# Kernel optimization log

Hardware: AMD Instinct MI355X
Metric: run time of the kernel (lower is better)

## Reference

```python
import jax, jax.numpy as jnp
import numpy as np

B, C, N = 8, 512, 4096
G = 8          # GroupNorm groups (8 <= C)
EPS = 1e-6


def setup_inputs() -> dict:
    key = jax.random.key(0)
    ks = jax.random.split(key, 5)
    return {
        "x": jax.random.normal(ks[0], (B, C, N), dtype=jnp.float32),
        "qkv_w": jax.random.normal(ks[1], (3 * C, C), dtype=jnp.float32) * (C ** -0.5),
        "qkv_b": jax.random.normal(ks[2], (3 * C,), dtype=jnp.float32) * 0.02,
        "proj_w": jax.random.normal(ks[3], (C, C), dtype=jnp.float32) * (C ** -0.5),
        "proj_b": jax.random.normal(ks[4], (C,), dtype=jnp.float32) * 0.02,
        "gn_scale": jnp.ones((C,), dtype=jnp.float32),
        "gn_bias": jnp.zeros((C,), dtype=jnp.float32),
    }


def group_norm(x, scale, bias):
    b, c, n = x.shape
    xr = x.reshape(b, G, c // G, n)
    mean = xr.mean(axis=(2, 3), keepdims=True)
    var = xr.var(axis=(2, 3), keepdims=True)
    h = ((xr - mean) * jax.lax.rsqrt(var + EPS)).reshape(b, c, n)
    return h * scale[None, :, None] + bias[None, :, None]


def reference(x, qkv_w, qkv_b, proj_w, proj_b, gn_scale, gn_bias):
    c = x.shape[1]
    h = group_norm(x, gn_scale, gn_bias)
    # 1x1 Conv1d == channel-mixing GEMM
    qkv = jnp.einsum('oc,bcn->bon', qkv_w, h) + qkv_b[None, :, None]
    q, k, v = jnp.split(qkv, 3, axis=1)           # each [B, C, N]
    q = q * (c ** -0.5)
    k = jax.nn.softmax(k, axis=-1)                # softmax over tokens
    # linear attention: context = k v^T over tokens, then project q
    context = jnp.einsum('bdn,ben->bde', k, v)    # [B, C, C]
    out = jnp.einsum('bde,bdn->ben', context, q)  # [B, C, N]
    y = jnp.einsum('oc,bcn->bon', proj_w, out) + proj_b[None, :, None]
    return x + y
```

## Files before the change

### kernel.cpp

```cpp
#include <hip/hip_runtime.h>

#define BB 8
#define CC 512
#define NT 4096
#define GG 8
#define CPG 64
#define EPSF 1e-6f
#define SQK 0.04419417382415922f

typedef __attribute__((ext_vector_type(8))) short bf16x8;
typedef __attribute__((ext_vector_type(4))) float f32x4;

#define OFF_RED  0
#define OFF_PB2  4096
#define OFF_IZ   270336
#define OFF_WKV  274432
#define OFF_PWB  536576
#define OFF_WQT  667648
#define OFF_MB   798720
#define OFF_PBF  1847296
#define OFF_CTXB 2895872
#define OFF_PCTX 3944448
#define OFF_HT   12333056
#define OFF_KVB  20721664

__device__ __forceinline__ ushort f2bf(float f) {
  union { float f; uint u; } v; v.f = f;
  uint r = (v.u + 0x7fffu + ((v.u >> 16) & 1u)) >> 16;
  return (ushort)r;
}
__device__ __forceinline__ float bf2f(ushort h) {
  union { uint u; float f; } v; v.u = ((uint)h) << 16;
  return v.f;
}
__device__ __forceinline__ uint pk(float a, float b) {
  return (uint)f2bf(a) | ((uint)f2bf(b) << 16);
}
__device__ __forceinline__ void gload16(const ushort* g, ushort* l) {
  __builtin_amdgcn_global_load_lds((const __attribute__((address_space(1))) void*)g,
                                   (__attribute__((address_space(3))) void*)l, 16, 0, 0);
}
#define KSWZ(kofs, row) ((kofs) ^ ((((row) >> 1) & 3) << 3))

__global__ __launch_bounds__(256) void gn_stats1(const float* __restrict__ x,
                                                 float* __restrict__ red) {
  int bg = blockIdx.y, chunk = blockIdx.x;
  const float4* p4 = (const float4*)(x + (size_t)bg * (CPG * NT) + (size_t)chunk * 32768);
  int tid = threadIdx.x;
  float s = 0.f, sq = 0.f;
  for (int i = tid; i < 8192; i += 256) {
    float4 v = p4[i];
    s  += v.x + v.y + v.z + v.w;
    sq += v.x * v.x + v.y * v.y + v.z * v.z + v.w * v.w;
  }
  for (int off = 32; off > 0; off >>= 1) {
    s  += __shfl_down(s, off);
    sq += __shfl_down(sq, off);
  }
  __shared__ float ls[4], lq[4];
  int wid = tid >> 6, lane = tid & 63;
  if (lane == 0) { ls[wid] = s; lq[wid] = sq; }
  __syncthreads();
  if (tid == 0) {
    red[(bg * 8 + chunk) * 2]     = ls[0] + ls[1] + ls[2] + ls[3];
    red[(bg * 8 + chunk) * 2 + 1] = lq[0] + lq[1] + lq[2] + lq[3];
  }
}

__global__ __launch_bounds__(256) void wconv2(const float* __restrict__ qkv_w,
                                              const float* __restrict__ proj_w,
                                              ushort* __restrict__ wkvb,
                                              ushort* __restrict__ pwb) {
  int bid = blockIdx.x;
  if (bid < 512) {
    int idx = (bid * 256 + threadIdx.x) * 4;
    float4 v = *(const float4*)(qkv_w + (size_t)CC * CC + idx);
    *(uint2*)(wkvb + idx) = make_uint2(pk(v.x, v.y), pk(v.z, v.w));
  } else {
    int idx = ((bid - 512) * 256 + threadIdx.x) * 4;
    float4 v = *(const float4*)(proj_w + idx);
    *(uint2*)(pwb + idx) = make_uint2(pk(v.x, v.y), pk(v.z, v.w));
  }
}

__global__ __launch_bounds__(256) void wqt_kernel(const float* __restrict__ qkv_w,
                                                  ushort* __restrict__ wqT) {
  __shared__ float t[32][33];
  int d0 = blockIdx.y * 32, c0 = blockIdx.x * 32;
  int tid = threadIdx.x;
  int r = tid >> 3, c4 = (tid & 7) * 4;
  float4 v = *(const float4*)(qkv_w + (size_t)(d0 + r) * CC + c0 + c4);
  t[r][c4] = v.x; t[r][c4 + 1] = v.y; t[r][c4 + 2] = v.z; t[r][c4 + 3] = v.w;
  __syncthreads();
  int r2 = tid >> 3, d4 = (tid & 7) * 4;
  uint w0 = pk(t[d4][r2], t[d4 + 1][r2]);
  uint w1 = pk(t[d4 + 2][r2], t[d4 + 3][r2]);
  *(uint2*)&wqT[(size_t)(c0 + r2) * CC + d0 + d4] = make_uint2(w0, w1);
}

__global__ __launch_bounds__(256) void ht_kernel(
    const float* __restrict__ x, const float* __restrict__ red,
    const float* __restrict__ gn_scale, const float* __restrict__ gn_bias,
    ushort* __restrict__ hT) {
  __shared__ float ts[64][68];
  __shared__ float la[64], lb[64];
  int b = blockIdx.z, g = blockIdx.y, n0 = blockIdx.x * 64;
  int c0 = g * 64;
  int tid = threadIdx.x;
  if (tid == 0) {
    int bg = b * 8 + g;
    float s = 0.f, sq = 0.f;
#pragma unroll
    for (int i = 0; i < 8; i++) {
      s  += red[(bg * 8 + i) * 2];
      sq += red[(bg * 8 + i) * 2 + 1];
    }
    float mean = s / (float)(CPG * NT);
    float var  = sq / (float)(CPG * NT) - mean * mean;
    ts[0][0] = mean; ts[0][1] = rsqrtf(var + EPSF);
  }
  __syncthreads();
  if (tid < 64) {
    float mean = ts[0][0], rstd = ts[0][1];
    float a = gn_scale[c0 + tid] * rstd;
    la[tid] = a;
    lb[tid] = gn_bias[c0 + tid] - mean * a;
  }
  __syncthreads();
  int tn = (tid & 15) * 4, tc = tid >> 4;
#pragma unroll
  for (int it = 0; it < 4; it++) {
    int c = tc + it * 16;
    float a  = la[c];
    float bb = lb[c];
    float4 v = *(const float4*)(x + ((size_t)(b * CC + c0 + c)) * NT + n0 + tn);
    ts[c][tn]     = a * v.x + bb;
    ts[c][tn + 1] = a * v.y + bb;
    ts[c][tn + 2] = a * v.z + bb;
    ts[c][tn + 3] = a * v.w + bb;
  }
  __syncthreads();
#pragma unroll
  for (int it = 0; it < 2; it++) {
    int idx = tid + it * 256;
    int n = idx >> 3, c8 = (idx & 7) * 8;
    uint w[4];
#pragma unroll
    for (int j = 0; j < 4; j++)
      w[j] = pk(ts[c8 + 2 * j][n], ts[c8 + 2 * j + 1][n]);
    *(uint4*)&hT[((size_t)b * NT + n0 + n) * CC + c0 + c8] = make_uint4(w[0], w[1], w[2], w[3]);
  }
}

#define TBUF 16384

__device__ __forceinline__ void stage256(const ushort* __restrict__ G, ushort* L,
                                         int LD, int wave, int lane) {
  int rw = wave * 8 + (lane >> 3);
  int cg = lane & 7;
#pragma unroll
  for (int s = 0; s < 4; s++) {
    int row = s * 64 + rw;
    int gcol = (cg ^ (row & 7)) * 8;
    gload16(G + (size_t)row * LD + gcol, L + s * 4096 + wave * 512);
  }
}

template <int NTILES>
__device__ __forceinline__ void mfma256(const ushort* __restrict__ A,
                                        const ushort* __restrict__ B,
                                        int LDA, int LDB, ushort* As, ushort* Bs,
                                        int tid, f32x4 acc[8][4]) {
  int wave = tid >> 6, lane = tid & 63;
  int wr = wave >> 2, wc = wave & 3;
  stage256(A, As, LDA, wave, lane);
  stage256(B, Bs, LDB, wave, lane);
  const ushort* gA = A + 64;
  const ushort* gB = B + 64;
  int rowA = wr * 128 + (lane & 15);
  int rowB = wc * 64 + (lane & 15);
  int kg0 = lane >> 4;
#pragma unroll 1
  for (int t = 0; t < NTILES; t++) {
    __builtin_amdgcn_s_barrier();
    asm volatile("" ::: "memory");
    if (t + 1 < NTILES) {
      stage256(gA, As + ((t + 1) & 1) * TBUF, LDA, wave, lane);
      stage256(gB, Bs + ((t + 1) & 1) * TBUF, LDB, wave, lane);
      gA += 64; gB += 64;
      asm volatile("s_waitcnt vmcnt(8)" ::: "memory");
    } else {
      asm volatile("s_waitcnt vmcnt(0)" ::: "memory");
    }
    __builtin_amdgcn_s_barrier();
    asm volatile("" ::: "memory");
    const ushort* Ab = As + (t & 1) * TBUF;
    const ushort* Bb = Bs + (t & 1) * TBUF;
#pragma unroll
    for (int kk = 0; kk < 2; kk++) {
      int kg = kg0 + kk * 4;
      bf16x8 bfr[4];
#pragma unroll
      for (int ni = 0; ni < 4; ni++) {
        int r = rowB + ni * 16;
        bfr[ni] = *(const bf16x8*)(Bb + r * 64 + ((kg ^ (r & 7)) << 3));
      }
#pragma unroll
      for (int mi = 0; mi < 8; mi++) {
        int r = rowA + mi * 16;
        bf16x8 afr = *(const bf16x8*)(Ab + r * 64 + ((kg ^ (r & 7)) << 3));
#pragma unroll
        for (int ni = 0; ni < 4; ni++)
          acc[mi][ni] = __builtin_amdgcn_mfma_f32_16x16x32_bf16(afr, bfr[ni], acc[mi][ni], 0, 0, 0);
      }
    }
  }
}

template <int KTOT, int LDA, int LDB>
__device__ __forceinline__ void mfma_loop64(const ushort* __restrict__ A,
                                            const ushort* __restrict__ B,
                                            ushort* As, ushort* Bs, int tid,
                                            f32x4 acc[2][2]) {
  int wave = tid >> 6, lane = tid & 63;
  int srow = tid >> 2;
  int kofs = KSWZ((tid & 3) * 8, srow & 15);
  const ushort* ga = A + (size_t)srow * LDA + kofs;
  const ushort* gb = B + (size_t)srow * LDB + kofs;
  int lo = wave * 512;
  int wm = (wave >> 1) * 32, wn = (wave & 1) * 32;
  int rowl = lane & 15;
  int kread = KSWZ((lane >> 4) * 8, rowl);
  int aoff = (wm + rowl) * 32 + kread;
  int boff = (wn + rowl) * 32 + kread;
  constexpr int NIT = KTOT / 32;
  gload16(ga, As + lo); gload16(gb, Bs + lo);
  ga += 32; gb += 32;
#pragma unroll 1
  for (int t = 0; t < NIT; t++) {
    int cb = (t & 1) * 2048;
    int nb = 2048 - cb;
    if (t + 1 < NIT) {
      gload16(ga, As + nb + lo); gload16(gb, Bs + nb + lo);
      ga += 32; gb += 32;
      asm volatile("s_waitcnt vmcnt(2)" ::: "memory");
    } else {
      asm volatile("s_waitcnt vmcnt(0)" ::: "memory");
    }
    __builtin_amdgcn_s_barrier();
    asm volatile("" ::: "memory");
    bf16x8 a[2], b[2];
#pragma unroll
    for (int m = 0; m < 2; m++) a[m] = *(const bf16x8*)(As + cb + aoff + m * 512);
#pragma unroll
    for (int n = 0; n < 2; n++) b[n] = *(const bf16x8*)(Bs + cb + boff + n * 512);
#pragma unroll
    for (int m = 0; m < 2; m++)
#pragma unroll
      for (int n = 0; n < 2; n++)
        acc[m][n] = __builtin_amdgcn_mfma_f32_16x16x32_bf16(a[m], b[n], acc[m][n], 0, 0, 0);
    asm volatile("" ::: "memory");
    __builtin_amdgcn_s_barrier();
    asm volatile("" ::: "memory");
  }
}

__global__ __launch_bounds__(512) void kv_gemm_bf16(
    const ushort* __restrict__ wkvb, const ushort* __restrict__ hT,
    const float* __restrict__ qkv_b, ushort* __restrict__ kvb) {
  extern __shared__ ushort lds[];
  ushort* As = lds;
  ushort* Bs = lds + 2 * TBUF;
  int b = blockIdx.z, n0 = blockIdx.x * 256, m0 = blockIdx.y * 256;
  int tid = threadIdx.x;
  f32x4 acc[8][4] = {{{0.f, 0.f, 0.f, 0.f}}};
  mfma256<8>(wkvb + (size_t)m0 * CC, hT + (size_t)b * NT * CC + (size_t)n0 * CC,
             CC, CC, As, Bs, tid, acc);
  int wave = tid >> 6, lane = tid & 63;
  int wr = wave >> 2, wc = wave & 3;
  int col = lane & 15, rb = (lane >> 4) * 4;
  bool isK = (m0 < 512);
#pragma unroll
  for (int mi = 0; mi < 8; mi++)
#pragma unroll
    for (int j = 0; j < 4; j++) {
      int gm = m0 + wr * 128 + mi * 16 + rb + j;
      float bias = qkv_b[CC + gm];
      ushort* orow = kvb + ((size_t)(b * 1024 + gm)) * NT + n0 + wc * 64 + col;
#pragma unroll
      for (int ni = 0; ni < 4; ni++) {
        float val = acc[mi][ni][j] + bias;
        if (isK) val = __expf(val);
        orow[ni * 16] = f2bf(val);
      }
    }
}

__global__ __launch_bounds__(256) void zred(const ushort* __restrict__ kvb,
                                            float* __restrict__ invZ) {
  int row = blockIdx.x;
  int b = row >> 9, d = row & 511;
  const ushort* p = kvb + ((size_t)(b * 1024 + d)) * NT;
  int tid = threadIdx.x;
  uint4 r0 = *(const uint4*)(p + tid * 16);
  uint4 r1 = *(const uint4*)(p + tid * 16 + 8);
  uint w[8] = {r0.x, r0.y, r0.z, r0.w, r1.x, r1.y, r1.z, r1.w};
  float s = 0.f;
#pragma unroll
  for (int i = 0; i < 8; i++) {
    union { uint u; float f; } lo, hi;
    lo.u = w[i] << 16; hi.u = w[i] & 0xffff0000u;
    s += lo.f + hi.f;
  }
  for (int off = 32; off > 0; off >>= 1) s += __shfl_down(s, off);
  __shared__ float red[4];
  int wid = tid >> 6, lane = tid & 63;
  if (lane == 0) red[wid] = s;
  __syncthreads();
  if (tid == 0) invZ[row] = 1.f / (red[0] + red[1] + red[2] + red[3]);
}

__global__ __launch_bounds__(512) void ctx_gemm_split(
    const ushort* __restrict__ kvb, ushort* __restrict__ pctx) {
  extern __shared__ ushort lds[];
  ushort* As = lds;
  ushort* Bs = lds + 2 * TBUF;
  int e0 = blockIdx.x * 256, d0 = blockIdx.y * 256;
  int bz = blockIdx.z, b = bz >> 3, s = bz & 7;
  int tid = threadIdx.x;
  f32x4 acc[8][4] = {{{0.f, 0.f, 0.f, 0.f}}};
  const ushort* K = kvb + (size_t)b * 1024 * NT + (size_t)d0 * NT + s * 512;
  const ushort* V = kvb + ((size_t)b * 1024 + 512) * NT + (size_t)e0 * NT + s * 512;
  mfma256<8>(K, V, NT, NT, As, Bs, tid, acc);
  int wave = tid >> 6, lane = tid & 63;
  int wr = wave >> 2, wc = wave & 3;
  int col = lane & 15, rb = (lane >> 4) * 4;
#pragma unroll
  for (int mi = 0; mi < 8; mi++)
#pragma unroll
    for (int j = 0; j < 4; j++) {
      int gd = d0 + wr * 128 + mi * 16 + rb + j;
      ushort* orow = pctx + ((size_t)(b * 8 + s) * CC + gd) * CC + e0 + wc * 64 + col;
#pragma unroll
      for (int ni = 0; ni < 4; ni++)
        orow[ni * 16] = f2bf(acc[mi][ni][j]);
    }
}

__global__ __launch_bounds__(256) void ctx_red(const ushort* __restrict__ pctx,
                                               const float* __restrict__ invZ,
                                               ushort* __restrict__ ctxb) {
  int t = blockIdx.x * 256 + threadIdx.x;
  int b = t >> 15;
  int r = (t & 32767) * 8;
  int d = r >> 9;
  float iz = invZ[b * 512 + d];
  const ushort* base = pctx + (size_t)b * 8 * 262144 + r;
  float f[8] = {};
#pragma unroll
  for (int s = 0; s < 8; s++) {
    uint4 v = *(const uint4*)(base + (size_t)s * 262144);
    uint w[4] = {v.x, v.y, v.z, v.w};
#pragma unroll
    for (int j = 0; j < 4; j++) {
      union { uint u; float f; } lo, hi;
      lo.u = w[j] << 16; hi.u = w[j] & 0xffff0000u;
      f[2 * j] += lo.f; f[2 * j + 1] += hi.f;
    }
  }
  uint o[4];
#pragma unroll
  for (int j = 0; j < 4; j++) o[j] = pk(f[2 * j] * iz, f[2 * j + 1] * iz);
  *(uint4*)(ctxb + (size_t)b * 262144 + r) = make_uint4(o[0], o[1], o[2], o[3]);
}

__global__ __launch_bounds__(256) void m_gemm_bf16(
    const ushort* __restrict__ pwb, const ushort* __restrict__ ctxb,
    ushort* __restrict__ Mb) {
  __shared__ ushort As[4096], Bs[4096];
  int b = blockIdx.z, d0 = blockIdx.x * 64, o0 = blockIdx.y * 64;
  int tid = threadIdx.x;
  f32x4 acc[2][2] = {{{0.f, 0.f, 0.f, 0.f}}};
  mfma_loop64<CC, CC, CC>(pwb + (size_t)o0 * CC,
                          ctxb + (size_t)b * CC * CC + (size_t)d0 * CC, As, Bs, tid, acc);
  int wave = tid >> 6, lane = tid & 63;
  int wm = (wave >> 1) * 32, wn = (wave & 1) * 32;
  int col = lane & 15, rb = (lane >> 4) * 4;
#pragma unroll
  for (int m = 0; m < 2; m++)
#pragma unroll
    for (int n = 0; n < 2; n++)
#pragma unroll
      for (int j = 0; j < 4; j++) {
        int go = o0 + wm + m * 16 + rb + j;
        int gd = d0 + wn + n * 16 + col;
        Mb[((size_t)b * CC + go) * CC + gd] = f2bf(acc[m][n][j] * SQK);
      }
}

__global__ __launch_bounds__(256) void p_gemm_bf16(
    const ushort* __restrict__ Mb, const ushort* __restrict__ wqT,
    ushort* __restrict__ Pb) {
  __shared__ ushort As[4096], Bs[4096];
  int b = blockIdx.z, c0 = blockIdx.x * 64, o0 = blockIdx.y * 64;
  int tid = threadIdx.x;
  f32x4 acc[2][2] = {{{0.f, 0.f, 0.f, 0.f}}};
  mfma_loop64<CC, CC, CC>(Mb + (size_t)b * CC * CC + (size_t)o0 * CC,
                          wqT + (size_t)c0 * CC, As, Bs, tid, acc);
  int wave = tid >> 6, lane = tid & 63;
  int wm = (wave >> 1) * 32, wn = (wave & 1) * 32;
  int col = lane & 15, rb = (lane >> 4) * 4;
#pragma unroll
  for (int m = 0; m < 2; m++)
#pragma unroll
    for (int n = 0; n < 2; n++)
#pragma unroll
      for (int j = 0; j < 4; j++) {
        int go = o0 + wm + m * 16 + rb + j;
        int gc = c0 + wn + n * 16 + col;
        Pb[((size_t)b * CC + go) * CC + gc] = f2bf(acc[m][n][j]);
      }
}

__global__ __launch_bounds__(256) void pb2_kernel(
    const ushort* __restrict__ Mb, const float* __restrict__ qkv_b,
    const float* __restrict__ proj_b, float* __restrict__ pb2) {
  int b = blockIdx.x, og = blockIdx.y;
  int r = og * 64 + (threadIdx.x >> 2);
  int q = threadIdx.x & 3;
  const ushort* Mr = Mb + ((size_t)(b * CC + r)) * CC + q * 128;
  const float* bq = qkv_b + q * 128;
  float s = 0.f;
#pragma unroll
  for (int i = 0; i < 16; i++) {
    uint4 v = *(const uint4*)(Mr + i * 8);
    uint w[4] = {v.x, v.y, v.z, v.w};
#pragma unroll
    for (int j = 0; j < 4; j++) {
      union { uint u; float f; } lo, hi;
      lo.u = w[j] << 16; hi.u = w[j] & 0xffff0000u;
      s += lo.f * bq[i * 8 + 2 * j] + hi.f * bq[i * 8 + 2 * j + 1];
    }
  }
  s += __shfl_xor(s, 1);
  s += __shfl_xor(s, 2);
  if (q == 0) pb2[b * CC + r] = s + proj_b[r];
}

__global__ __launch_bounds__(512) void final_gemm_bf16(
    const float* __restrict__ x, const ushort* __restrict__ Pb,
    const ushort* __restrict__ hT, const float* __restrict__ pb2,
    float* __restrict__ out) {
  extern __shared__ ushort lds[];
  ushort* As = lds;
  ushort* Bs = lds + 2 * TBUF;
  int b = blockIdx.z, n0 = blockIdx.x * 256, m0 = blockIdx.y * 256;
  int tid = threadIdx.x;
  f32x4 acc[8][4] = {{{0.f, 0.f, 0.f, 0.f}}};
  mfma256<8>(Pb + (size_t)b * CC * CC + (size_t)m0 * CC,
             hT + (size_t)b * NT * CC + (size_t)n0 * CC, CC, CC, As, Bs, tid, acc);
  int wave = tid >> 6, lane = tid & 63;
  int wr = wave >> 2, wc = wave & 3;
  int col = lane & 15, rb = (lane >> 4) * 4;
#pragma unroll
  for (int mi = 0; mi < 8; mi++)
#pragma unroll
    for (int j = 0; j < 4; j++) {
      int gm = m0 + wr * 128 + mi * 16 + rb + j;
      float bias = pb2[b * CC + gm];
      size_t rowoff = ((size_t)(b * CC + gm)) * NT + n0 + wc * 64 + col;
#pragma unroll
      for (int ni = 0; ni < 4; ni++)
        out[rowoff + ni * 16] = acc[mi][ni][j] + bias + x[rowoff + ni * 16];
    }
}

extern "C" void kernel_launch(void* const* d_in, const int* in_sizes, int n_in,
                              void* d_out, int out_size, void* d_ws, size_t ws_size,
                              hipStream_t stream) {
  const float* x        = (const float*)d_in[0];
  const float* qkv_w    = (const float*)d_in[1];
  const float* qkv_b    = (const float*)d_in[2];
  const float* proj_w   = (const float*)d_in[3];
  const float* proj_b   = (const float*)d_in[4];
  const float* gn_scale = (const float*)d_in[5];
  const float* gn_bias  = (const float*)d_in[6];
  float* out = (float*)d_out;
  float* ws  = (float*)d_ws;

  float*  red   = ws + OFF_RED;
  float*  pb2   = ws + OFF_PB2;
  float*  invZ  = ws + OFF_IZ;
  ushort* wkvb  = (ushort*)(ws + OFF_WKV);
  ushort* pwb   = (ushort*)(ws + OFF_PWB);
  ushort* wqT   = (ushort*)(ws + OFF_WQT);
  ushort* Mb    = (ushort*)(ws + OFF_MB);
  ushort* Pb    = (ushort*)(ws + OFF_PBF);
  ushort* ctxb  = (ushort*)(ws + OFF_CTXB);
  ushort* pctx  = (ushort*)(ws + OFF_PCTX);
  ushort* hT    = (ushort*)(ws + OFF_HT);
  ushort* kvb   = (ushort*)(ws + OFF_KVB);

  constexpr int DSM = 4 * TBUF * 2;
  static bool attr_set = false;
  (void)attr_set;
  hipFuncSetAttribute((const void*)kv_gemm_bf16,
                      hipFuncAttributeMaxDynamicSharedMemorySize, DSM);
  hipFuncSetAttribute((const void*)ctx_gemm_split,
                      hipFuncAttributeMaxDynamicSharedMemorySize, DSM);
  hipFuncSetAttribute((const void*)final_gemm_bf16,
                      hipFuncAttributeMaxDynamicSharedMemorySize, DSM);

  gn_stats1<<<dim3(8, 64), 256, 0, stream>>>(x, red);
  wconv2<<<768, 256, 0, stream>>>(qkv_w, proj_w, wkvb, pwb);
  wqt_kernel<<<dim3(16, 16), 256, 0, stream>>>(qkv_w, wqT);
  ht_kernel<<<dim3(64, 8, 8), 256, 0, stream>>>(x, red, gn_scale, gn_bias, hT);
  kv_gemm_bf16<<<dim3(16, 4, 8), 512, DSM, stream>>>(wkvb, hT, qkv_b, kvb);
  zred<<<4096, 256, 0, stream>>>(kvb, invZ);
  ctx_gemm_split<<<dim3(2, 2, 64), 512, DSM, stream>>>(kvb, pctx);
  ctx_red<<<1024, 256, 0, stream>>>(pctx, invZ, ctxb);
  m_gemm_bf16<<<dim3(8, 8, 8), 256, 0, stream>>>(pwb, ctxb, Mb);
  p_gemm_bf16<<<dim3(8, 8, 8), 256, 0, stream>>>(Mb, wqT, Pb);
  pb2_kernel<<<dim3(8, 8), 256, 0, stream>>>(Mb, qkv_b, proj_b, pb2);
  final_gemm_bf16<<<dim3(16, 2, 8), 512, DSM, stream>>>(x, Pb, hT, pb2, out);
}
```

Baseline: 194.6 us.

## Restructure 256-tile MFMA loop into four phases interleaving prefetch with compute

Splits each K-tile of the 256x256 bf16 MFMA main loop into four quadrant phases. Each phase loads its LDS fragments, issues part of the next tile's global-to-LDS prefetch in the first two phases, then runs a burst of MFMAs at raised wave priority between scheduling barriers. The goal is to spread global loads across the compute and overlap them with MFMA issue, in the style of ping-pong scheduling, instead of issuing all loads up front and waiting. The cost is more barriers per tile (two per phase) and fragments being reloaded per phase, which could add synchronisation overhead.

```diff
diff --git a/kernel.cpp b/kernel.cpp
--- a/kernel.cpp
+++ b/kernel.cpp
@@ -154,16 +154,14 @@
 
 #define TBUF 16384
 
-__device__ __forceinline__ void stage256(const ushort* __restrict__ G, ushort* L,
-                                         int LD, int wave, int lane) {
+__device__ __forceinline__ void stage_sweep(const ushort* __restrict__ G,
+                                            ushort* L, int LD, int wave,
+                                            int lane, int s) {
   int rw = wave * 8 + (lane >> 3);
   int cg = lane & 7;
-#pragma unroll
-  for (int s = 0; s < 4; s++) {
-    int row = s * 64 + rw;
-    int gcol = (cg ^ (row & 7)) * 8;
-    gload16(G + (size_t)row * LD + gcol, L + s * 4096 + wave * 512);
-  }
+  int row = s * 64 + rw;
+  int gcol = (cg ^ (row & 7)) * 8;
+  gload16(G + (size_t)row * LD + gcol, L + s * 4096 + wave * 512);
 }
 
 template <int NTILES>
@@ -173,46 +171,69 @@
                                         int tid, f32x4 acc[8][4]) {
   int wave = tid >> 6, lane = tid & 63;
   int wr = wave >> 2, wc = wave & 3;
-  stage256(A, As, LDA, wave, lane);
-  stage256(B, Bs, LDB, wave, lane);
+#pragma unroll
+  for (int s = 0; s < 4; s++) {
+    stage_sweep(A, As, LDA, wave, lane, s);
+    stage_sweep(B, Bs, LDB, wave, lane, s);
+  }
   const ushort* gA = A + 64;
   const ushort* gB = B + 64;
+  asm volatile("s_waitcnt vmcnt(0)" ::: "memory");
+  __builtin_amdgcn_s_barrier();
   int rowA = wr * 128 + (lane & 15);
   int rowB = wc * 64 + (lane & 15);
   int kg0 = lane >> 4;
 #pragma unroll 1
   for (int t = 0; t < NTILES; t++) {
-    __builtin_amdgcn_s_barrier();
-    asm volatile("" ::: "memory");
-    if (t + 1 < NTILES) {
-      stage256(gA, As + ((t + 1) & 1) * TBUF, LDA, wave, lane);
-      stage256(gB, Bs + ((t + 1) & 1) * TBUF, LDB, wave, lane);
-      gA += 64; gB += 64;
-      asm volatile("s_waitcnt vmcnt(8)" ::: "memory");
-    } else {
-      asm volatile("s_waitcnt vmcnt(0)" ::: "memory");
-    }
-    __builtin_amdgcn_s_barrier();
-    asm volatile("" ::: "memory");
     const ushort* Ab = As + (t & 1) * TBUF;
     const ushort* Bb = Bs + (t & 1) * TBUF;
-#pragma unroll
-    for (int kk = 0; kk < 2; kk++) {
-      int kg = kg0 + kk * 4;
-      bf16x8 bfr[4];
-#pragma unroll
-      for (int ni = 0; ni < 4; ni++) {
-        int r = rowB + ni * 16;
-        bfr[ni] = *(const bf16x8*)(Bb + r * 64 + ((kg ^ (r & 7)) << 3));
+    ushort* An = As + ((t + 1) & 1) * TBUF;
+    ushort* Bn = Bs + ((t + 1) & 1) * TBUF;
+    bool pf = (t + 1 < NTILES);
+#pragma unroll
+    for (int ph = 0; ph < 4; ph++) {
+      int qm = ph >> 1, qn = ph & 1;
+      bf16x8 afr[2][4], bfr[2][2];
+#pragma unroll
+      for (int kk = 0; kk < 2; kk++) {
+        int kg = kg0 + kk * 4;
+#pragma unroll
+        for (int i = 0; i < 4; i++) {
+          int r = rowA + (qm * 4 + i) * 16;
+          afr[kk][i] = *(const bf16x8*)(Ab + r * 64 + ((kg ^ (r & 7)) << 3));
+        }
+#pragma unroll
+        for (int i = 0; i < 2; i++) {
+          int r = rowB + (qn * 2 + i) * 16;
+          bfr[kk][i] = *(const bf16x8*)(Bb + r * 64 + ((kg ^ (r & 7)) << 3));
+        }
       }
-#pragma unroll
-      for (int mi = 0; mi < 8; mi++) {
-        int r = rowA + mi * 16;
-        bf16x8 afr = *(const bf16x8*)(Ab + r * 64 + ((kg ^ (r & 7)) << 3));
-#pragma unroll
-        for (int ni = 0; ni < 4; ni++)
-          acc[mi][ni] = __builtin_amdgcn_mfma_f32_16x16x32_bf16(afr, bfr[ni], acc[mi][ni], 0, 0, 0);
+      if (pf && ph < 2) {
+        stage_sweep(gA, An, LDA, wave, lane, ph * 2);
+        stage_sweep(gA, An, LDA, wave, lane, ph * 2 + 1);
+        stage_sweep(gB, Bn, LDB, wave, lane, ph * 2);
+        stage_sweep(gB, Bn, LDB, wave, lane, ph * 2 + 1);
       }
+      __builtin_amdgcn_s_barrier();
+      asm volatile("s_waitcnt lgkmcnt(0)" ::: "memory");
+      __builtin_amdgcn_sched_barrier(0);
+      __builtin_amdgcn_s_setprio(1);
+#pragma unroll
+      for (int kk = 0; kk < 2; kk++)
+#pragma unroll
+        for (int i = 0; i < 4; i++)
+#pragma unroll
+          for (int jn = 0; jn < 2; jn++)
+            acc[qm * 4 + i][qn * 2 + jn] = __builtin_amdgcn_mfma_f32_16x16x32_bf16(
+                afr[kk][i], bfr[kk][jn], acc[qm * 4 + i][qn * 2 + jn], 0, 0, 0);
+      __builtin_amdgcn_s_setprio(0);
+      __builtin_amdgcn_sched_barrier(0);
+      if (ph == 3 && pf) {
+        asm volatile("s_waitcnt vmcnt(0)" ::: "memory");
+        gA += 64; gB += 64;
+      }
+      __builtin_amdgcn_s_barrier();
+      asm volatile("" ::: "memory");
     }
   }
 }
@@ -502,8 +523,6 @@
   ushort* kvb   = (ushort*)(ws + OFF_KVB);
 
   constexpr int DSM = 4 * TBUF * 2;
-  static bool attr_set = false;
-  (void)attr_set;
   hipFuncSetAttribute((const void*)kv_gemm_bf16,
                       hipFuncAttributeMaxDynamicSharedMemorySize, DSM);
   hipFuncSetAttribute((const void*)ctx_gemm_split,
```

Measured after the change: 204.2 us. 1.05x slower.
